# Kernel optimization log

Measured on AMD Instinct MI355X. Metric: run time of the kernel, lower is better.

## Reference

```python
import jax, jax.numpy as jnp
import numpy as np
from jax import lax

KH, KW, K = 3, 3, 9
PAD, BN_EPS = 1, 1e-5


def setup_inputs() -> dict:
    key = jax.random.key(0)
    ks = jax.random.split(key, 10)
    B, CHI, CHO, H, W = 2, 64, 64, 128, 128
    x = jax.random.normal(ks[0], (B, CHI, H, W), dtype=jnp.float32)
    # offset/mask branch conv: 3*K output channels (o1, o2, mask)
    w_off = jax.random.normal(ks[1], (3 * K, CHI, KH, KW), dtype=jnp.float32) * 0.01
    b_off = jax.random.normal(ks[2], (3 * K,), dtype=jnp.float32) * 0.01
    # main deformable conv weight/bias
    fan = CHI * K
    weight = jax.random.normal(ks[3], (CHO, CHI, KH, KW), dtype=jnp.float32) / np.sqrt(fan)
    bias = jax.random.normal(ks[4], (CHO,), dtype=jnp.float32) * 0.01
    # BatchNorm (eval-mode) params
    gamma = jax.random.uniform(ks[5], (CHO,), minval=0.5, maxval=1.5, dtype=jnp.float32)
    beta = jax.random.normal(ks[6], (CHO,), dtype=jnp.float32) * 0.1
    run_mean = jax.random.normal(ks[7], (CHO,), dtype=jnp.float32) * 0.1
    run_var = jax.random.uniform(ks[8], (CHO,), minval=0.5, maxval=1.5, dtype=jnp.float32)
    return {"x": x, "w_off": w_off, "b_off": b_off, "weight": weight,
            "bias": bias, "gamma": gamma, "beta": beta,
            "run_mean": run_mean, "run_var": run_var}


def _dcn_bn_relu(x, w_off, b_off, weight, bias, gamma, beta, run_mean, run_var):
    B, C, H, W = x.shape
    CHO = weight.shape[0]
    # offset/mask branch: regular 3x3 conv, stride 1, pad 1
    om = lax.conv_general_dilated(
        x, w_off, window_strides=(1, 1), padding=[(PAD, PAD), (PAD, PAD)],
        dimension_numbers=("NCHW", "OIHW", "NCHW")) + b_off[None, :, None, None]
    o1, o2, m = jnp.split(om, 3, axis=1)          # each [B, K, H, W]
    offset = jnp.concatenate([o1, o2], axis=1)    # [B, 2K, H, W]
    off_y = offset[:, 0::2]                       # interleaved (y, x) per tap, as in DCNv2 CUDA
    off_x = offset[:, 1::2]
    mask = jax.nn.sigmoid(m)                      # [B, K, H, W] modulation

    # sampling positions: p = p0 + p_k + offset
    ky, kx = jnp.meshgrid(jnp.arange(KH), jnp.arange(KW), indexing="ij")
    ky = ky.reshape(K).astype(x.dtype)
    kx = kx.reshape(K).astype(x.dtype)
    hh = jnp.arange(H, dtype=x.dtype)
    ww = jnp.arange(W, dtype=x.dtype)
    py = hh[None, None, :, None] - PAD + ky[None, :, None, None] + off_y  # [B,K,H,W]
    px = ww[None, None, None, :] - PAD + kx[None, :, None, None] + off_x

    y0f = jnp.floor(py)
    x0f = jnp.floor(px)
    ly = (py - y0f)[..., None]
    lx = (px - x0f)[..., None]
    y0 = y0f.astype(jnp.int32)
    x0 = x0f.astype(jnp.int32)
    bidx = jnp.arange(B)[:, None, None, None]

    def gather(yi, xi):
        valid = ((yi >= 0) & (yi < H) & (xi >= 0) & (xi < W)).astype(x.dtype)
        yc = jnp.clip(yi, 0, H - 1)
        xc = jnp.clip(xi, 0, W - 1)
        g = x[bidx, :, yc, xc]                    # [B, K, H, W, C]
        return g * valid[..., None]

    v00 = gather(y0, x0)
    v01 = gather(y0, x0 + 1)
    v10 = gather(y0 + 1, x0)
    v11 = gather(y0 + 1, x0 + 1)
    sampled = (v00 * (1 - ly) * (1 - lx) + v01 * (1 - ly) * lx
               + v10 * ly * (1 - lx) + v11 * ly * lx)
    sampled = sampled * mask[..., None]           # modulated

    out = jnp.einsum("bkhwc,ock->bohw", sampled,
                     weight.reshape(CHO, C, K)) + bias[None, :, None, None]

    # eval-mode BatchNorm + ReLU
    inv = gamma / jnp.sqrt(run_var + BN_EPS)
    out = (out - run_mean[None, :, None, None]) * inv[None, :, None, None] \
          + beta[None, :, None, None]
    return jax.nn.relu(out)


def reference(x, w_off, b_off, weight, bias, gamma, beta, run_mean, run_var):
    return _dcn_bn_relu(x, w_off, b_off, weight, bias, gamma, beta, run_mean, run_var)
```

## Files before the change

### kernel.cpp

```cpp
#include <hip/hip_runtime.h>
#include <hip/hip_bf16.h>

#define HH 128
#define WW 128
#define CI 64
#define CO 64
#define SLS 584
#define HPS 72
#define HALW 18
#define TS 18688

typedef __attribute__((ext_vector_type(8))) short short8;
typedef __attribute__((ext_vector_type(4))) float floatx4;

__device__ __forceinline__ unsigned short f2bf(float f) {
  union { float f; unsigned u; } uu; uu.f = f;
  unsigned r = uu.u + 0x7FFFu + ((uu.u >> 16) & 1u);
  return (unsigned short)(r >> 16);
}
__device__ __forceinline__ unsigned pack2bf(float lo, float hi) {
  return (unsigned)f2bf(lo) | ((unsigned)f2bf(hi) << 16);
}
__device__ __forceinline__ float bfl(unsigned u) { return __uint_as_float(u << 16); }
__device__ __forceinline__ float bfh(unsigned u) { return __uint_as_float(u & 0xffff0000u); }

__global__ __launch_bounds__(256) void prep_kernel(
    const float* __restrict__ x, unsigned* __restrict__ xTb_u,
    const float* __restrict__ weight, const float* __restrict__ bias,
    const float* __restrict__ gamma, const float* __restrict__ beta,
    const float* __restrict__ mean, const float* __restrict__ var,
    const float* __restrict__ w_off, const float* __restrict__ b_off,
    unsigned short* __restrict__ Wm, unsigned short* __restrict__ w2,
    float* __restrict__ bias2, float* __restrict__ boff2) {
  __shared__ unsigned T2[32 * 33];
  int bid = blockIdx.x;
  int tid = threadIdx.x;
  if (bid < 1024) {
    int b = bid >> 9, h = (bid >> 2) & 127, q = bid & 3;
    int cp = tid >> 3, wc = tid & 7;
    const float* xp = x + (((long)(b * CI + 2 * cp) * HH + h) * WW + q * 32 + wc * 4);
    float4 a0 = *(const float4*)xp;
    float4 a1 = *(const float4*)(xp + HH * WW);
    T2[(wc * 4 + 0) * 33 + cp] = pack2bf(a0.x, a1.x);
    T2[(wc * 4 + 1) * 33 + cp] = pack2bf(a0.y, a1.y);
    T2[(wc * 4 + 2) * 33 + cp] = pack2bf(a0.z, a1.z);
    T2[(wc * 4 + 3) * 33 + cp] = pack2bf(a0.w, a1.w);
    __syncthreads();
    int px = tid >> 3, g = tid & 7;
    const unsigned* src = &T2[px * 33 + g * 4];
    unsigned* dst = xTb_u + ((long)((b * HH + h) * WW + q * 32 + px)) * 32 + g * 4;
    *(uint4*)dst = make_uint4(src[0], src[1], src[2], src[3]);
    return;
  }
  int idx = (bid - 1024) * 256 + tid;
  if (idx < 32) boff2[idx] = (idx < 27) ? b_off[idx] : 0.f;
  if (idx >= CO * 576) return;
  int o = idx / 576, kc = idx - o * 576;
  int k = kc >> 6, c = kc & 63;
  float inv = gamma[o] * rsqrtf(var[o] + 1e-5f);
  Wm[idx] = f2bf(weight[(o * CI + c) * 9 + k] * inv);
  if (kc == 0) bias2[o] = (bias[o] - mean[o]) * inv + beta[o];
  if (o < 27) w2[idx] = f2bf(w_off[o * 576 + c * 9 + k]);
  else if (o < 32) w2[idx] = 0;
}

__global__ __launch_bounds__(256, 4) void dcn_kernel(
    const unsigned short* __restrict__ xTb,
    const unsigned short* __restrict__ w2, const float* __restrict__ boff2,
    const unsigned short* __restrict__ Wm, const float* __restrict__ bias2,
    float* __restrict__ out) {
  __shared__ char smem[2 * TS];

  int bid = blockIdx.x;
  int s = bid & 7;
  int n = bid >> 3;
  int b = n >> 6;
  int rem = n & 63;
  int h = s * 16 + (rem >> 2);
  int w00 = (rem & 3) * 32;
  int tid = threadIdx.x, lane = tid & 63, wave = tid >> 6;

#pragma unroll
  for (int it = 0; it < 4; it++) {
    int t = it * 256 + tid;
    if (t < 864) {
      int ti = (t >= 432);
      int tt = t - ti * 432;
      int row = tt / 144;
      int r2 = tt - row * 144;
      int xi = r2 >> 3, cg = r2 & 7;
      int y = h - 1 + row, xx = w00 + ti * 16 - 1 + xi;
      uint4 v = make_uint4(0u, 0u, 0u, 0u);
      if ((unsigned)y < (unsigned)HH && (unsigned)xx < (unsigned)WW)
        v = *(const uint4*)(xTb + (long)((b * HH + y) * WW + xx) * CI + cg * 8);
      short* hal = (short*)(smem + ti * TS);
      *(uint4*)(hal + (row * HALW + xi) * HPS + cg * 8) = v;
    }
  }
  __syncthreads();

  {
    int r16 = lane & 15, quad = lane >> 4;
    int m16 = wave & 1, kh = wave >> 1;
#pragma unroll
    for (int ti = 0; ti < 2; ti++) {
      short* hal = (short*)(smem + ti * TS);
      float* omL = (float*)(smem + ti * TS + 14016);
      floatx4 t0 = {0.f, 0.f, 0.f, 0.f};
      floatx4 t1 = {0.f, 0.f, 0.f, 0.f};
      if (kh == 0) t0 = *(const floatx4*)(boff2 + m16 * 16 + quad * 4);
      const short* ap = (const short*)(w2 + (m16 * 16 + r16) * 576 + kh * 32 + quad * 8);
#pragma unroll
      for (int kk = 0; kk < 9; kk++) {
        int dy = kk / 3, dxk = kk - 3 * dy;
        short8 bfrag = *(const short8*)(hal + (dy * HALW + r16 + dxk) * HPS + kh * 32 + quad * 8);
        short8 afrag = *(const short8*)(ap + kk * 64);
        if (kk & 1)
          t1 = __builtin_amdgcn_mfma_f32_16x16x32_bf16(afrag, bfrag, t1, 0, 0, 0);
        else
          t0 = __builtin_amdgcn_mfma_f32_16x16x32_bf16(afrag, bfrag, t0, 0, 0, 0);
      }
      floatx4 t = t0 + t1;
      *(floatx4*)(omL + kh * 576 + r16 * 36 + m16 * 16 + quad * 4) = t;
    }
  }
  __syncthreads();

  float pwx[2] = {0.f, 0.f}, pwy[2] = {0.f, 0.f}, pwz[2] = {0.f, 0.f}, pww[2] = {0.f, 0.f};
  int pov[2] = {0, 0};
  if (lane < 36) {
    int p_loc = (lane * 7282) >> 16;
    int k = lane - p_loc * 9;
    int p = wave * 4 + p_loc;
    int ky = (k * 11) >> 5;
    int kx = k - 3 * ky;
#pragma unroll
    for (int ti = 0; ti < 2; ti++) {
      const float* omL = (const float*)(smem + ti * TS + 14016);
      int w0 = w00 + ti * 16;
      const float* o0 = omL + p * 36;
      const float* o1 = omL + 576 + p * 36;
      float oy = o0[2 * k] + o1[2 * k];
      float ox = o0[2 * k + 1] + o1[2 * k + 1];
      float mm = o0[18 + k] + o1[18 + k];
      float msk = 1.f / (1.f + __expf(-mm));
      float py = (float)(h - 1 + ky) + oy;
      float pxx = (float)(w0 + p - 1 + kx) + ox;
      float y0f = floorf(py), x0f = floorf(pxx);
      float ly = py - y0f, lx = pxx - x0f;
      int y0 = (int)y0f, x0 = (int)x0f;
      int y1 = y0 + 1, x1 = x0 + 1;
      float lylx = ly * lx;
      bool y0v = (unsigned)y0 < (unsigned)HH, y1v = (unsigned)y1 < (unsigned)HH;
      bool x0v = (unsigned)x0 < (unsigned)WW, x1v = (unsigned)x1 < (unsigned)WW;
      int yc0 = min(max(y0, 0), HH - 1), yc1 = min(max(y1, 0), HH - 1);
      int xc0 = min(max(x0, 0), WW - 1), xc1 = min(max(x1, 0), WW - 1);
      pwx[ti] = (y0v && x0v) ? (1.f - ly - lx + lylx) * msk : 0.f;
      pwy[ti] = (y0v && x1v) ? (lx - lylx) * msk : 0.f;
      pwz[ti] = (y1v && x0v) ? (ly - lylx) * msk : 0.f;
      pww[ti] = (y1v && x1v) ? lylx * msk : 0.f;
      int off00 = (yc0 * WW + xc0) * CI;
      int dxs = (xc1 - xc0) * CI;
      int dys = (yc1 - yc0) * WW * CI;
      pov[ti] = off00 | ((dxs >> 6) << 20) | ((dys >> 13) << 21);
    }
  }
  __syncthreads();

  {
    int cq = lane & 15, pl = lane >> 4;
    int p = wave * 4 + pl;
    int ch = cq * 4;
    const unsigned short* xb = xTb + (long)b * (HH * WW * CI);
    uint2 uA[3][4], uB[2][4], uC[2][4], uD[2][4];

#define LOADK(U, kk)                                  \
    {                                                 \
      int v = povr[kk];                               \
      int o00 = (v & 0xFFFFF) + ch;                   \
      int dxv = (v >> 14) & 64;                       \
      int dyv = (v >> 8) & 8192;                      \
      U[0] = *(const uint2*)(xb + o00);               \
      U[1] = *(const uint2*)(xb + o00 + dxv);         \
      U[2] = *(const uint2*)(xb + o00 + dyv);         \
      U[3] = *(const uint2*)(xb + o00 + dyv + dxv);   \
    }

#define COMBK(U, kk)                                                                          \
    {                                                                                         \
      int src = pl * 9 + (kk);                                                                \
      float wx = __shfl(pwxt, src), wy = __shfl(pwyt, src);                                   \
      float wz = __shfl(pwzt, src), ww = __shfl(pwwt, src);                                   \
      float lo0 = bfl(U[0].x) * wx + bfl(U[1].x) * wy + bfl(U[2].x) * wz + bfl(U[3].x) * ww;  \
      float hi0 = bfh(U[0].x) * wx + bfh(U[1].x) * wy + bfh(U[2].x) * wz + bfh(U[3].x) * ww;  \
      float lo1 = bfl(U[0].y) * wx + bfl(U[1].y) * wy + bfl(U[2].y) * wz + bfl(U[3].y) * ww;  \
      float hi1 = bfh(U[0].y) * wx + bfh(U[1].y) * wy + bfh(U[2].y) * wz + bfh(U[3].y) * ww;  \
      unsigned r0, r1;                                                                        \
      asm("v_cvt_pk_bf16_f32 %0, %1, %2" : "=v"(r0) : "v"(lo0), "v"(hi0));                    \
      asm("v_cvt_pk_bf16_f32 %0, %1, %2" : "=v"(r1) : "v"(lo1), "v"(hi1));                    \
      *(uint2*)(&SL[p * SLS + (kk) * 64 + ch]) = make_uint2(r0, r1);                          \
    }

#pragma unroll
    for (int ti = 0; ti < 2; ti++) {
      __hip_bfloat16* SL = (__hip_bfloat16*)(smem + ti * TS);
      float pwxt = pwx[ti], pwyt = pwy[ti], pwzt = pwz[ti], pwwt = pww[ti];
      int povr[9];
#pragma unroll
      for (int k = 0; k < 9; k++) povr[k] = __shfl(pov[ti], pl * 9 + k);
      LOADK(uA[0], 0) LOADK(uA[1], 1) LOADK(uA[2], 2)
      LOADK(uB[0], 3) LOADK(uB[1], 4)
      COMBK(uA[0], 0) COMBK(uA[1], 1) COMBK(uA[2], 2)
      LOADK(uC[0], 5) LOADK(uC[1], 6)
      COMBK(uB[0], 3) COMBK(uB[1], 4)
      LOADK(uD[0], 7) LOADK(uD[1], 8)
      COMBK(uC[0], 5) COMBK(uC[1], 6)
      COMBK(uD[0], 7) COMBK(uD[1], 8)
    }
#undef LOADK
#undef COMBK
  }
  __syncthreads();

  {
    int r16 = lane & 15, quad = lane >> 4;
    floatx4 binit = *(const floatx4*)(bias2 + wave * 16 + quad * 4);
    const unsigned short* Ap = Wm + (wave * 16 + r16) * 576 + quad * 8;
#pragma unroll
    for (int ti = 0; ti < 2; ti++) {
      const __hip_bfloat16* SL = (const __hip_bfloat16*)(smem + ti * TS);
      const __hip_bfloat16* Sp = &SL[r16 * SLS + quad * 8];
      floatx4 acc0 = binit;
      floatx4 acc1 = {0.f, 0.f, 0.f, 0.f};
#pragma unroll
      for (int kc0 = 0; kc0 < 576; kc0 += 64) {
        short8 av0 = *(const short8*)(Ap + kc0);
        short8 bv0 = *(const short8*)(Sp + kc0);
        acc0 = __builtin_amdgcn_mfma_f32_16x16x32_bf16(av0, bv0, acc0, 0, 0, 0);
        short8 av1 = *(const short8*)(Ap + kc0 + 32);
        short8 bv1 = *(const short8*)(Sp + kc0 + 32);
        acc1 = __builtin_amdgcn_mfma_f32_16x16x32_bf16(av1, bv1, acc1, 0, 0, 0);
      }
      floatx4 acc = acc0 + acc1;
#pragma unroll
      for (int r = 0; r < 4; r++) {
        int o = wave * 16 + quad * 4 + r;
        out[((b * CO + o) * HH + h) * WW + w00 + ti * 16 + r16] = fmaxf(acc[r], 0.f);
      }
    }
  }
}

extern "C" void kernel_launch(void* const* d_in, const int* in_sizes, int n_in,
                              void* d_out, int out_size, void* d_ws, size_t ws_size,
                              hipStream_t stream) {
  const float* x = (const float*)d_in[0];
  const float* w_off = (const float*)d_in[1];
  const float* b_off = (const float*)d_in[2];
  const float* weight = (const float*)d_in[3];
  const float* bias = (const float*)d_in[4];
  const float* gamma = (const float*)d_in[5];
  const float* beta = (const float*)d_in[6];
  const float* run_mean = (const float*)d_in[7];
  const float* run_var = (const float*)d_in[8];
  float* outp = (float*)d_out;

  char* ws = (char*)d_ws;
  unsigned* xTb = (unsigned*)ws;
  unsigned short* Wm = (unsigned short*)(ws + 4194304);
  unsigned short* w2 = (unsigned short*)(ws + 4268032);
  float* bias2 = (float*)(ws + 4304896);
  float* boff2 = (float*)(ws + 4305152);

  prep_kernel<<<1168, 256, 0, stream>>>(x, xTb, weight, bias, gamma, beta,
                                        run_mean, run_var, w_off, b_off,
                                        Wm, w2, bias2, boff2);
  dcn_kernel<<<1024, 256, 0, stream>>>((const unsigned short*)xTb, w2, boff2,
                                       Wm, bias2, outp);
}
```

Baseline: 108.9 us.

## Overlap second-tile gather with first-tile MFMA and fold weight prep into transpose blocks

The main kernel now interleaves the bilinear gather loads and combines for the second 16-pixel tile with the MFMA GEMM of the first tile, so global-memory latency overlaps with matrix work. This adds a barrier and keeps more loaded values live in registers, which may raise register pressure at four blocks per CU. Separately, the weight/bias prep work is spread over the existing 1024 transpose blocks, 36 threads each, removing the 144 extra prep blocks. Per-tile offset shuffles are hoisted before the first barrier.

```diff
diff --git a/kernel.cpp b/kernel.cpp
--- a/kernel.cpp
+++ b/kernel.cpp
@@ -35,7 +35,7 @@
   __shared__ unsigned T2[32 * 33];
   int bid = blockIdx.x;
   int tid = threadIdx.x;
-  if (bid < 1024) {
+  {
     int b = bid >> 9, h = (bid >> 2) & 127, q = bid & 3;
     int cp = tid >> 3, wc = tid & 7;
     const float* xp = x + (((long)(b * CI + 2 * cp) * HH + h) * WW + q * 32 + wc * 4);
@@ -50,18 +50,18 @@
     const unsigned* src = &T2[px * 33 + g * 4];
     unsigned* dst = xTb_u + ((long)((b * HH + h) * WW + q * 32 + px)) * 32 + g * 4;
     *(uint4*)dst = make_uint4(src[0], src[1], src[2], src[3]);
-    return;
-  }
-  int idx = (bid - 1024) * 256 + tid;
-  if (idx < 32) boff2[idx] = (idx < 27) ? b_off[idx] : 0.f;
-  if (idx >= CO * 576) return;
-  int o = idx / 576, kc = idx - o * 576;
-  int k = kc >> 6, c = kc & 63;
-  float inv = gamma[o] * rsqrtf(var[o] + 1e-5f);
-  Wm[idx] = f2bf(weight[(o * CI + c) * 9 + k] * inv);
-  if (kc == 0) bias2[o] = (bias[o] - mean[o]) * inv + beta[o];
-  if (o < 27) w2[idx] = f2bf(w_off[o * 576 + c * 9 + k]);
-  else if (o < 32) w2[idx] = 0;
+  }
+  if (tid < 36) {
+    int idx = bid * 36 + tid;
+    if (idx < 32) boff2[idx] = (idx < 27) ? b_off[idx] : 0.f;
+    int o = idx / 576, kc = idx - o * 576;
+    int k = kc >> 6, c = kc & 63;
+    float inv = gamma[o] * rsqrtf(var[o] + 1e-5f);
+    Wm[idx] = f2bf(weight[(o * CI + c) * 9 + k] * inv);
+    if (kc == 0) bias2[o] = (bias[o] - mean[o]) * inv + beta[o];
+    if (o < 27) w2[idx] = f2bf(w_off[o * 576 + c * 9 + k]);
+    else if (o < 32) w2[idx] = 0;
+  }
 }
 
 __global__ __launch_bounds__(256, 4) void dcn_kernel(
@@ -165,18 +165,22 @@
       pov[ti] = off00 | ((dxs >> 6) << 20) | ((dys >> 13) << 21);
     }
   }
-  __syncthreads();
-
-  {
-    int cq = lane & 15, pl = lane >> 4;
-    int p = wave * 4 + pl;
-    int ch = cq * 4;
-    const unsigned short* xb = xTb + (long)b * (HH * WW * CI);
-    uint2 uA[3][4], uB[2][4], uC[2][4], uD[2][4];
-
-#define LOADK(U, kk)                                  \
+  int cq = lane & 15, pl = lane >> 4;
+  int p = wave * 4 + pl;
+  int ch = cq * 4;
+  int povrX[9], povrY[9];
+#pragma unroll
+  for (int k = 0; k < 9; k++) {
+    povrX[k] = __shfl(pov[0], pl * 9 + k);
+    povrY[k] = __shfl(pov[1], pl * 9 + k);
+  }
+  __syncthreads();
+
+  const unsigned short* xb = xTb + (long)b * (HH * WW * CI);
+
+#define LOADK(U, kk, PV)                              \
     {                                                 \
-      int v = povr[kk];                               \
+      int v = PV[kk];                                 \
       int o00 = (v & 0xFFFFF) + ch;                   \
       int dxv = (v >> 14) & 64;                       \
       int dyv = (v >> 8) & 8192;                      \
@@ -186,11 +190,11 @@
       U[3] = *(const uint2*)(xb + o00 + dyv + dxv);   \
     }
 
-#define COMBK(U, kk)                                                                          \
+#define COMBK(U, kk, SLP, PX, PY, PZ, PW)                                                     \
     {                                                                                         \
       int src = pl * 9 + (kk);                                                                \
-      float wx = __shfl(pwxt, src), wy = __shfl(pwyt, src);                                   \
-      float wz = __shfl(pwzt, src), ww = __shfl(pwwt, src);                                   \
+      float wx = __shfl(PX, src), wy = __shfl(PY, src);                                       \
+      float wz = __shfl(PZ, src), ww = __shfl(PW, src);                                       \
       float lo0 = bfl(U[0].x) * wx + bfl(U[1].x) * wy + bfl(U[2].x) * wz + bfl(U[3].x) * ww;  \
       float hi0 = bfh(U[0].x) * wx + bfh(U[1].x) * wy + bfh(U[2].x) * wz + bfh(U[3].x) * ww;  \
       float lo1 = bfl(U[0].y) * wx + bfl(U[1].y) * wy + bfl(U[2].y) * wz + bfl(U[3].y) * ww;  \
@@ -198,27 +202,27 @@
       unsigned r0, r1;                                                                        \
       asm("v_cvt_pk_bf16_f32 %0, %1, %2" : "=v"(r0) : "v"(lo0), "v"(hi0));                    \
       asm("v_cvt_pk_bf16_f32 %0, %1, %2" : "=v"(r1) : "v"(lo1), "v"(hi1));                    \
-      *(uint2*)(&SL[p * SLS + (kk) * 64 + ch]) = make_uint2(r0, r1);                          \
-    }
-
-#pragma unroll
-    for (int ti = 0; ti < 2; ti++) {
-      __hip_bfloat16* SL = (__hip_bfloat16*)(smem + ti * TS);
-      float pwxt = pwx[ti], pwyt = pwy[ti], pwzt = pwz[ti], pwwt = pww[ti];
-      int povr[9];
-#pragma unroll
-      for (int k = 0; k < 9; k++) povr[k] = __shfl(pov[ti], pl * 9 + k);
-      LOADK(uA[0], 0) LOADK(uA[1], 1) LOADK(uA[2], 2)
-      LOADK(uB[0], 3) LOADK(uB[1], 4)
-      COMBK(uA[0], 0) COMBK(uA[1], 1) COMBK(uA[2], 2)
-      LOADK(uC[0], 5) LOADK(uC[1], 6)
-      COMBK(uB[0], 3) COMBK(uB[1], 4)
-      LOADK(uD[0], 7) LOADK(uD[1], 8)
-      COMBK(uC[0], 5) COMBK(uC[1], 6)
-      COMBK(uD[0], 7) COMBK(uD[1], 8)
-    }
-#undef LOADK
-#undef COMBK
+      *(uint2*)(&SLP[p * SLS + (kk) * 64 + ch]) = make_uint2(r0, r1);                         \
+    }
+
+  __hip_bfloat16* SLX = (__hip_bfloat16*)smem;
+  __hip_bfloat16* SLY = (__hip_bfloat16*)(smem + TS);
+
+  {
+    uint2 uA[3][4], uB[2][4], uC[2][4], uD[2][4];
+    LOADK(uA[0], 0, povrX) LOADK(uA[1], 1, povrX) LOADK(uA[2], 2, povrX)
+    LOADK(uB[0], 3, povrX) LOADK(uB[1], 4, povrX)
+    COMBK(uA[0], 0, SLX, pwx[0], pwy[0], pwz[0], pww[0])
+    COMBK(uA[1], 1, SLX, pwx[0], pwy[0], pwz[0], pww[0])
+    COMBK(uA[2], 2, SLX, pwx[0], pwy[0], pwz[0], pww[0])
+    LOADK(uC[0], 5, povrX) LOADK(uC[1], 6, povrX)
+    COMBK(uB[0], 3, SLX, pwx[0], pwy[0], pwz[0], pww[0])
+    COMBK(uB[1], 4, SLX, pwx[0], pwy[0], pwz[0], pww[0])
+    LOADK(uD[0], 7, povrX) LOADK(uD[1], 8, povrX)
+    COMBK(uC[0], 5, SLX, pwx[0], pwy[0], pwz[0], pww[0])
+    COMBK(uC[1], 6, SLX, pwx[0], pwy[0], pwz[0], pww[0])
+    COMBK(uD[0], 7, SLX, pwx[0], pwy[0], pwz[0], pww[0])
+    COMBK(uD[1], 8, SLX, pwx[0], pwy[0], pwz[0], pww[0])
   }
   __syncthreads();
 
@@ -226,29 +230,74 @@
     int r16 = lane & 15, quad = lane >> 4;
     floatx4 binit = *(const floatx4*)(bias2 + wave * 16 + quad * 4);
     const unsigned short* Ap = Wm + (wave * 16 + r16) * 576 + quad * 8;
-#pragma unroll
-    for (int ti = 0; ti < 2; ti++) {
-      const __hip_bfloat16* SL = (const __hip_bfloat16*)(smem + ti * TS);
-      const __hip_bfloat16* Sp = &SL[r16 * SLS + quad * 8];
-      floatx4 acc0 = binit;
-      floatx4 acc1 = {0.f, 0.f, 0.f, 0.f};
-#pragma unroll
-      for (int kc0 = 0; kc0 < 576; kc0 += 64) {
-        short8 av0 = *(const short8*)(Ap + kc0);
-        short8 bv0 = *(const short8*)(Sp + kc0);
-        acc0 = __builtin_amdgcn_mfma_f32_16x16x32_bf16(av0, bv0, acc0, 0, 0, 0);
-        short8 av1 = *(const short8*)(Ap + kc0 + 32);
-        short8 bv1 = *(const short8*)(Sp + kc0 + 32);
-        acc1 = __builtin_amdgcn_mfma_f32_16x16x32_bf16(av1, bv1, acc1, 0, 0, 0);
-      }
-      floatx4 acc = acc0 + acc1;
-#pragma unroll
-      for (int r = 0; r < 4; r++) {
-        int o = wave * 16 + quad * 4 + r;
-        out[((b * CO + o) * HH + h) * WW + w00 + ti * 16 + r16] = fmaxf(acc[r], 0.f);
-      }
-    }
-  }
+    const __hip_bfloat16* Sp = &SLX[r16 * SLS + quad * 8];
+    uint2 vA[5][4], vB[4][4];
+    LOADK(vA[0], 0, povrY) LOADK(vA[1], 1, povrY) LOADK(vA[2], 2, povrY)
+    LOADK(vA[3], 3, povrY) LOADK(vA[4], 4, povrY)
+    floatx4 acc0 = binit;
+    floatx4 acc1 = {0.f, 0.f, 0.f, 0.f};
+#pragma unroll
+    for (int kc0 = 0; kc0 < 256; kc0 += 64) {
+      short8 av0 = *(const short8*)(Ap + kc0);
+      short8 bv0 = *(const short8*)(Sp + kc0);
+      acc0 = __builtin_amdgcn_mfma_f32_16x16x32_bf16(av0, bv0, acc0, 0, 0, 0);
+      short8 av1 = *(const short8*)(Ap + kc0 + 32);
+      short8 bv1 = *(const short8*)(Sp + kc0 + 32);
+      acc1 = __builtin_amdgcn_mfma_f32_16x16x32_bf16(av1, bv1, acc1, 0, 0, 0);
+    }
+    COMBK(vA[0], 0, SLY, pwx[1], pwy[1], pwz[1], pww[1])
+    COMBK(vA[1], 1, SLY, pwx[1], pwy[1], pwz[1], pww[1])
+    COMBK(vA[2], 2, SLY, pwx[1], pwy[1], pwz[1], pww[1])
+    COMBK(vA[3], 3, SLY, pwx[1], pwy[1], pwz[1], pww[1])
+    COMBK(vA[4], 4, SLY, pwx[1], pwy[1], pwz[1], pww[1])
+    LOADK(vB[0], 5, povrY) LOADK(vB[1], 6, povrY)
+    LOADK(vB[2], 7, povrY) LOADK(vB[3], 8, povrY)
+#pragma unroll
+    for (int kc0 = 256; kc0 < 576; kc0 += 64) {
+      short8 av0 = *(const short8*)(Ap + kc0);
+      short8 bv0 = *(const short8*)(Sp + kc0);
+      acc0 = __builtin_amdgcn_mfma_f32_16x16x32_bf16(av0, bv0, acc0, 0, 0, 0);
+      short8 av1 = *(const short8*)(Ap + kc0 + 32);
+      short8 bv1 = *(const short8*)(Sp + kc0 + 32);
+      acc1 = __builtin_amdgcn_mfma_f32_16x16x32_bf16(av1, bv1, acc1, 0, 0, 0);
+    }
+    COMBK(vB[0], 5, SLY, pwx[1], pwy[1], pwz[1], pww[1])
+    COMBK(vB[1], 6, SLY, pwx[1], pwy[1], pwz[1], pww[1])
+    COMBK(vB[2], 7, SLY, pwx[1], pwy[1], pwz[1], pww[1])
+    COMBK(vB[3], 8, SLY, pwx[1], pwy[1], pwz[1], pww[1])
+    floatx4 acc = acc0 + acc1;
+#pragma unroll
+    for (int r = 0; r < 4; r++) {
+      int o = wave * 16 + quad * 4 + r;
+      out[((b * CO + o) * HH + h) * WW + w00 + r16] = fmaxf(acc[r], 0.f);
+    }
+  }
+  __syncthreads();
+
+  {
+    int r16 = lane & 15, quad = lane >> 4;
+    floatx4 acc0 = *(const floatx4*)(bias2 + wave * 16 + quad * 4);
+    floatx4 acc1 = {0.f, 0.f, 0.f, 0.f};
+    const unsigned short* Ap = Wm + (wave * 16 + r16) * 576 + quad * 8;
+    const __hip_bfloat16* Sp = &SLY[r16 * SLS + quad * 8];
+#pragma unroll
+    for (int kc0 = 0; kc0 < 576; kc0 += 64) {
+      short8 av0 = *(const short8*)(Ap + kc0);
+      short8 bv0 = *(const short8*)(Sp + kc0);
+      acc0 = __builtin_amdgcn_mfma_f32_16x16x32_bf16(av0, bv0, acc0, 0, 0, 0);
+      short8 av1 = *(const short8*)(Ap + kc0 + 32);
+      short8 bv1 = *(const short8*)(Sp + kc0 + 32);
+      acc1 = __builtin_amdgcn_mfma_f32_16x16x32_bf16(av1, bv1, acc1, 0, 0, 0);
+    }
+    floatx4 acc = acc0 + acc1;
+#pragma unroll
+    for (int r = 0; r < 4; r++) {
+      int o = wave * 16 + quad * 4 + r;
+      out[((b * CO + o) * HH + h) * WW + w00 + 16 + r16] = fmaxf(acc[r], 0.f);
+    }
+  }
+#undef LOADK
+#undef COMBK
 }
 
 extern "C" void kernel_launch(void* const* d_in, const int* in_sizes, int n_in,
@@ -272,7 +321,7 @@
   float* bias2 = (float*)(ws + 4304896);
   float* boff2 = (float*)(ws + 4305152);
 
-  prep_kernel<<<1168, 256, 0, stream>>>(x, xTb, weight, bias, gamma, beta,
+  prep_kernel<<<1024, 256, 0, stream>>>(x, xTb, weight, bias, gamma, beta,
                                         run_mean, run_var, w_off, b_off,
                                         Wm, w2, bias2, boff2);
   dcn_kernel<<<1024, 256, 0, stream>>>((const unsigned short*)xTb, w2, boff2,
```

Measured after the change: 109.4 us. About the same (+0.5%).
